# Optimization experiments

Measured on AMD Instinct MI355X. Metric: run time of the kernel, lower is better.

Reference implementation:

```python
import jax, jax.numpy as jnp
import numpy as np

NA, NW = 131072, 131072
N = NA + NW
E = 1048576
R = 4
DIN = 64
H = 128
L = 2
EPS = 1e-5


def setup_inputs() -> dict:
    key = jax.random.key(0)
    ks = jax.random.split(key, 20)
    s_in = 1.0 / np.sqrt(DIN)
    s_h = 1.0 / np.sqrt(H)
    return {
        "x_assignments": jax.random.normal(ks[0], (NA, DIN), jnp.float32),
        "x_workers": jax.random.normal(ks[1], (NW, DIN), jnp.float32),
        "edge_index": jax.random.randint(ks[2], (2, E), 0, N),
        "edge_type": jax.random.randint(ks[3], (E,), 0, R),
        "W_in_a": jax.random.normal(ks[4], (DIN, H), jnp.float32) * s_in,
        "b_in_a": jnp.zeros((H,), jnp.float32),
        "W_in_w": jax.random.normal(ks[5], (DIN, H), jnp.float32) * s_in,
        "b_in_w": jnp.zeros((H,), jnp.float32),
        "W_rel": jax.random.normal(ks[6], (L, R, H, H), jnp.float32) * s_h,
        "W_root": jax.random.normal(ks[7], (L, H, H), jnp.float32) * s_h,
        "b_conv": jnp.zeros((L, H), jnp.float32),
        "ln_g": jnp.ones((L, H), jnp.float32),
        "ln_b": jnp.zeros((L, H), jnp.float32),
        "W_out": jax.random.normal(ks[8], (H, 1), jnp.float32) * s_h,
        "b_out": jnp.zeros((1,), jnp.float32),
        "base": jnp.zeros((), jnp.float32),
    }


def _layernorm(x, g, b):
    mu = jnp.mean(x, axis=-1, keepdims=True)
    var = jnp.var(x, axis=-1, keepdims=True)
    return (x - mu) * jax.lax.rsqrt(var + EPS) * g + b


def reference(x_assignments, x_workers, edge_index, edge_type,
              W_in_a, b_in_a, W_in_w, b_in_w,
              W_rel, W_root, b_conv, ln_g, ln_b,
              W_out, b_out, base):
    # type-specific input projection + relu, then flatten node space
    ha = jax.nn.relu(x_assignments @ W_in_a + b_in_a)
    hw = jax.nn.relu(x_workers @ W_in_w + b_in_w)
    h = jnp.concatenate([ha, hw], axis=0)  # [N, H]
    src, dst = edge_index[0], edge_index[1]
    for l in range(L):
        hs = h[src]  # [E, H] gathered source features
        out = h @ W_root[l] + b_conv[l]  # root transform + bias
        for r in range(R):
            m = (edge_type == r).astype(h.dtype)  # [E]
            agg = jax.ops.segment_sum(hs * m[:, None], dst, num_segments=N)
            cnt = jax.ops.segment_sum(m, dst, num_segments=N)
            mean = agg / jnp.maximum(cnt, 1.0)[:, None]  # per-relation mean aggr
            out = out + mean @ W_rel[l, r]
        h = jax.nn.relu(_layernorm(out, ln_g[l], ln_b[l]))
        # dropout inactive (eval mode)
    h_t = h[:NA]  # target node type slice (offset 0)
    pred = base + (h_t @ W_out + b_out)[:, 0]
    return pred
```

## Files before the change

### kernel.cpp

```cpp
#include <hip/hip_runtime.h>

#define NA_ 131072
#define NN  262144
#define EE  1048576
#define RR  4
#define EPS_ 1e-5f

typedef unsigned short ushort_t;
typedef unsigned char uchar_t;
typedef unsigned int uint_t;
typedef __attribute__((ext_vector_type(8))) short bf16x8;
typedef __attribute__((ext_vector_type(4))) float f32x4;

__device__ __forceinline__ float bf2f(uint_t u16) {
    return __uint_as_float(u16 << 16);
}
__device__ __forceinline__ uint_t f2bf(float f) {
    uint_t x = __float_as_uint(f);
    return (x + 0x7fffu + ((x >> 16) & 1u)) >> 16;
}

__device__ __forceinline__ void gl2lds16(const void* g, void* l) {
    __builtin_amdgcn_global_load_lds(
        (const __attribute__((address_space(1))) void*)g,
        (__attribute__((address_space(3))) void*)l, 16, 0, 0);
}

__global__ __launch_bounds__(256) void proj_gemm(const float* __restrict__ A,
                                                 const short* __restrict__ Btg,
                                                 const float* __restrict__ bias,
                                                 ushort_t* __restrict__ C) {
    const int K = 64;
    __shared__ short As[128][K + 8];
    __shared__ short Bs[128][K + 8];
    const int tid  = threadIdx.x;
    const int lane = tid & 63;
    const int l15  = lane & 15;
    const int q    = lane >> 4;
    const int wv   = tid >> 6;
    const int wr   = (wv >> 1) * 64;
    const int wc   = (wv & 1) * 64;
    const size_t blockRow = (size_t)blockIdx.x * 128;

    #pragma unroll
    for (int it = 0; it < 4; it++) {
        int sidx = (it * 256 + tid) * 8;
        int row = sidx / K, col = sidx % K;
        const float* Ag = A + (blockRow + row) * K + col;
        float4 v0 = *(const float4*)Ag;
        float4 v1 = *(const float4*)(Ag + 4);
        uint4 u;
        u.x = f2bf(v0.x) | (f2bf(v0.y) << 16);
        u.y = f2bf(v0.z) | (f2bf(v0.w) << 16);
        u.z = f2bf(v1.x) | (f2bf(v1.y) << 16);
        u.w = f2bf(v1.z) | (f2bf(v1.w) << 16);
        *(uint4*)&As[row][col] = u;
        *(uint4*)&Bs[row][col] = *(const uint4*)(Btg + (size_t)row * K + col);
    }
    __syncthreads();

    f32x4 acc[4][4];
    #pragma unroll
    for (int i = 0; i < 4; i++)
        #pragma unroll
        for (int j = 0; j < 4; j++) {
            acc[i][j][0] = 0.f; acc[i][j][1] = 0.f;
            acc[i][j][2] = 0.f; acc[i][j][3] = 0.f;
        }

    #pragma unroll
    for (int kk = 0; kk < 2; kk++) {
        bf16x8 af[4], bfr[4];
        #pragma unroll
        for (int i = 0; i < 4; i++)
            af[i] = *(const bf16x8*)&As[wr + i * 16 + l15][kk * 32 + q * 8];
        #pragma unroll
        for (int j = 0; j < 4; j++)
            bfr[j] = *(const bf16x8*)&Bs[wc + j * 16 + l15][kk * 32 + q * 8];
        #pragma unroll
        for (int i = 0; i < 4; i++)
            #pragma unroll
            for (int j = 0; j < 4; j++)
                acc[i][j] = __builtin_amdgcn_mfma_f32_16x16x32_bf16(
                    af[i], bfr[j], acc[i][j], 0, 0, 0);
    }

    #pragma unroll
    for (int j = 0; j < 4; j++) {
        int gcol = wc + j * 16 + l15;
        float bv = bias[gcol];
        #pragma unroll
        for (int i = 0; i < 4; i++) {
            size_t rbase = blockRow + wr + i * 16 + q * 4;
            #pragma unroll
            for (int r = 0; r < 4; r++) {
                float v = fmaxf(acc[i][j][r] + bv, 0.f);
                C[(rbase + r) * 128 + gcol] = (ushort_t)f2bf(v);
            }
        }
    }
}

__global__ void prep_weights(const float* __restrict__ Wia,
                             const float* __restrict__ Wiw,
                             const float* __restrict__ Wroot,
                             const float* __restrict__ Wrel,
                             short* __restrict__ wt) {
    int e = blockIdx.x * 256 + threadIdx.x;
    if (e < 8192) {
        int k = e >> 7, n = e & 127;
        wt[n * 64 + k] = (short)f2bf(Wia[e]);
    } else if (e < 16384) {
        int t = e - 8192;
        int k = t >> 7, n = t & 127;
        wt[8192 + n * 64 + k] = (short)f2bf(Wiw[t]);
    } else {
        int t = e - 16384;
        int l = t / 81920;
        int d = t % 81920;
        int kc = d / 16384;
        int rem2 = d % 16384;
        int n = rem2 >> 7;
        int kkk = rem2 & 127;
        float val = (kc < 4)
            ? Wrel[(((size_t)l * 4 + kc) * 128 + kkk) * 128 + n]
            : Wroot[((size_t)l * 128 + kkk) * 128 + n];
        wt[16384 + (size_t)l * 81920 + kc * 16384 + n * 128 + kkk] =
            (short)f2bf(val);
    }
}

__global__ void count_edges(const int* __restrict__ dstv,
                            const int* __restrict__ et,
                            uint_t* __restrict__ cntp,
                            uchar_t* __restrict__ rank) {
    int base = blockIdx.x * 1024 + threadIdx.x;
    int e0 = base, e1 = base + 256, e2 = base + 512, e3 = base + 768;
    int r0 = et[e0], r1 = et[e1], r2 = et[e2], r3 = et[e3];
    int d0 = dstv[e0], d1 = dstv[e1], d2 = dstv[e2], d3 = dstv[e3];
    uint_t o0 = atomicAdd(&cntp[(size_t)d0 * 16], 1u << (8 * r0));
    uint_t o1 = atomicAdd(&cntp[(size_t)d1 * 16], 1u << (8 * r1));
    uint_t o2 = atomicAdd(&cntp[(size_t)d2 * 16], 1u << (8 * r2));
    uint_t o3 = atomicAdd(&cntp[(size_t)d3 * 16], 1u << (8 * r3));
    rank[e0] = (uchar_t)((o0 >> (8 * r0)) & 0xffu);
    rank[e1] = (uchar_t)((o1 >> (8 * r1)) & 0xffu);
    rank[e2] = (uchar_t)((o2 >> (8 * r2)) & 0xffu);
    rank[e3] = (uchar_t)((o3 >> (8 * r3)) & 0xffu);
}

__global__ void inv_deg(const uint_t* __restrict__ cntp,
                        float* __restrict__ inv,
                        int* __restrict__ deg,
                        uint_t* __restrict__ prefd) {
    int i = blockIdx.x * 256 + threadIdx.x;
    if (i < NN) {
        uint_t c = cntp[(size_t)i * 16];
        int c0 = c & 255, c1 = (c >> 8) & 255, c2 = (c >> 16) & 255, c3 = c >> 24;
        float4 w;
        w.x = 1.0f / (float)(c0 > 1 ? c0 : 1);
        w.y = 1.0f / (float)(c1 > 1 ? c1 : 1);
        w.z = 1.0f / (float)(c2 > 1 ? c2 : 1);
        w.w = 1.0f / (float)(c3 > 1 ? c3 : 1);
        ((float4*)inv)[i] = w;
        deg[i] = c0 + c1 + c2 + c3;
        prefd[i] = ((uint_t)c0 << 8) | ((uint_t)(c0 + c1) << 16)
                 | ((uint_t)(c0 + c1 + c2) << 24);
    }
}

__global__ void scan1(const int* __restrict__ deg, int* __restrict__ offs,
                      int* __restrict__ bsum) {
    __shared__ int lds[256];
    int tid = threadIdx.x;
    int i = blockIdx.x * 256 + tid;
    int v = deg[i];
    int incl = v;
    lds[tid] = incl;
    __syncthreads();
    for (int off = 1; off < 256; off <<= 1) {
        int t = (tid >= off) ? lds[tid - off] : 0;
        __syncthreads();
        incl += t;
        lds[tid] = incl;
        __syncthreads();
    }
    offs[i] = incl - v;
    if (tid == 255) bsum[blockIdx.x] = incl;
}

__global__ void scan_bsum(int* __restrict__ bsum) {
    __shared__ int lds[256];
    int tid = threadIdx.x;
    int t0 = bsum[tid * 4 + 0], t1 = bsum[tid * 4 + 1];
    int t2 = bsum[tid * 4 + 2], t3 = bsum[tid * 4 + 3];
    int s = t0 + t1 + t2 + t3;
    int incl = s;
    lds[tid] = incl;
    __syncthreads();
    for (int off = 1; off < 256; off <<= 1) {
        int t = (tid >= off) ? lds[tid - off] : 0;
        __syncthreads();
        incl += t;
        lds[tid] = incl;
        __syncthreads();
    }
    int e = incl - s;
    bsum[tid * 4 + 0] = e;
    bsum[tid * 4 + 1] = e + t0;
    bsum[tid * 4 + 2] = e + t0 + t1;
    bsum[tid * 4 + 3] = e + t0 + t1 + t2;
}

__global__ void scan_add(int* __restrict__ offs, const int* __restrict__ bsum) {
    int i = blockIdx.x * 256 + threadIdx.x;
    offs[i] = offs[i] + bsum[blockIdx.x];
    if (i == 0) offs[NN] = EE;
}

__global__ void place_edges(const int* __restrict__ srcv,
                            const int* __restrict__ dstv,
                            const int* __restrict__ et,
                            const uchar_t* __restrict__ rank,
                            const int* __restrict__ offs,
                            const uint_t* __restrict__ prefd,
                            uint_t* __restrict__ pk) {
    int base = blockIdx.x * 1024 + threadIdx.x;
    #pragma unroll
    for (int t = 0; t < 4; t++) {
        int e = base + t * 256;
        int d = dstv[e], r = et[e];
        int pos = offs[d] + (int)((prefd[d] >> (8 * r)) & 255u) + (int)rank[e];
        pk[pos] = (uint_t)srcv[e] | ((uint_t)r << 18);
    }
}

__global__ __launch_bounds__(256) void agg_means(const uint_t* __restrict__ pk,
                                                 const int* __restrict__ offs,
                                                 const ushort_t* __restrict__ hold,
                                                 const float* __restrict__ inv,
                                                 ushort_t* __restrict__ M,
                                                 int lo, int rowsCap) {
    const int wv  = __builtin_amdgcn_readfirstlane(threadIdx.x >> 6);
    const int idx = blockIdx.x * 4 + wv;
    const int d   = lo + idx;
    const int lane = threadIdx.x & 63;
    const int beg = offs[d];
    const int end = offs[d + 1];
    const float4 w4 = ((const float4*)inv)[d];

    float a0x = 0.f, a0y = 0.f, a1x = 0.f, a1y = 0.f;
    float a2x = 0.f, a2y = 0.f, a3x = 0.f, a3y = 0.f;

    const uint_t* hold32 = (const uint_t*)hold;

    auto accs = [&](uint_t p, uint_t v, bool valid) {
        float x = bf2f(v & 0xffffu), y = bf2f(v >> 16);
        uint_t r = p >> 18;
        float m0 = (valid && r == 0u) ? 1.f : 0.f;
        float m1 = (valid && r == 1u) ? 1.f : 0.f;
        float m2 = (valid && r == 2u) ? 1.f : 0.f;
        float m3 = (valid && r == 3u) ? 1.f : 0.f;
        a0x += m0 * x;  a0y += m0 * y;
        a1x += m1 * x;  a1y += m1 * y;
        a2x += m2 * x;  a2y += m2 * y;
        a3x += m3 * x;  a3y += m3 * y;
    };

    for (int e = beg; e < end; e += 8) {
        const int last = end - 1;
        int a1i = (e + 1 < end) ? e + 1 : last;
        int a2i = (e + 2 < end) ? e + 2 : last;
        int a3i = (e + 3 < end) ? e + 3 : last;
        uint_t p0 = pk[e];
        uint_t p1 = pk[a1i];
        uint_t p2 = pk[a2i];
        uint_t p3 = pk[a3i];
        uint_t v0 = hold32[(size_t)(p0 & 0x3FFFFu) * 64 + lane];
        uint_t v1 = hold32[(size_t)(p1 & 0x3FFFFu) * 64 + lane];
        uint_t v2 = hold32[(size_t)(p2 & 0x3FFFFu) * 64 + lane];
        uint_t v3 = hold32[(size_t)(p3 & 0x3FFFFu) * 64 + lane];

        const bool hB = (e + 4 < end);
        if (hB) {
            int b1i = (e + 5 < end) ? e + 5 : last;
            int b2i = (e + 6 < end) ? e + 6 : last;
            int b3i = (e + 7 < end) ? e + 7 : last;
            uint_t q0 = pk[e + 4];
            uint_t q1 = pk[b1i];
            uint_t q2 = pk[b2i];
            uint_t q3 = pk[b3i];
            uint_t u0 = hold32[(size_t)(q0 & 0x3FFFFu) * 64 + lane];
            uint_t u1 = hold32[(size_t)(q1 & 0x3FFFFu) * 64 + lane];
            uint_t u2 = hold32[(size_t)(q2 & 0x3FFFFu) * 64 + lane];
            uint_t u3 = hold32[(size_t)(q3 & 0x3FFFFu) * 64 + lane];
            accs(p0, v0, true);
            accs(p1, v1, true);
            accs(p2, v2, true);
            accs(p3, v3, true);
            accs(q0, u0, true);
            accs(q1, u1, e + 5 < end);
            accs(q2, u2, e + 6 < end);
            accs(q3, u3, e + 7 < end);
        } else {
            accs(p0, v0, true);
            accs(p1, v1, e + 1 < end);
            accs(p2, v2, e + 2 < end);
            accs(p3, v3, e + 3 < end);
        }
    }

    uint_t* P = (uint_t*)M;
    size_t planeU = (size_t)rowsCap * 64;
    size_t rowU = (size_t)idx * 64 + lane;
    P[rowU]              = f2bf(a0x * w4.x) | (f2bf(a0y * w4.x) << 16);
    P[planeU + rowU]     = f2bf(a1x * w4.y) | (f2bf(a1y * w4.y) << 16);
    P[2 * planeU + rowU] = f2bf(a2x * w4.z) | (f2bf(a2y * w4.z) << 16);
    P[3 * planeU + rowU] = f2bf(a3x * w4.w) | (f2bf(a3y * w4.w) << 16);
}

template<bool HEAD>
__global__ __launch_bounds__(256) void layer_gemm_ln(
    const ushort_t* __restrict__ Mg,
    const ushort_t* __restrict__ hold,
    const short* __restrict__ Btg,
    const float* __restrict__ bconv,
    const float* __restrict__ lng,
    const float* __restrict__ lnb,
    ushort_t* __restrict__ hnew,
    const float* __restrict__ Wout,
    const float* __restrict__ bout,
    const float* __restrict__ basep,
    float* __restrict__ pred,
    int lo, int rowsCap) {
    __shared__ short As[64 * 128];
    __shared__ short Bs[128 * 128];
    __shared__ float lds_s[64][2], lds_q[64][2], lds_h[64][2];

    const int tid  = threadIdx.x;
    const int lane = tid & 63;
    const int l15  = lane & 15;
    const int q    = lane >> 4;
    const int wv   = tid >> 6;
    const int wr   = (wv >> 1) * 32;
    const int wc   = (wv & 1) * 64;
    const int blockRowL = blockIdx.x * 64;
    const size_t planeS = (size_t)rowsCap * 128;

    f32x4 acc[2][4];
    #pragma unroll
    for (int i = 0; i < 2; i++)
        #pragma unroll
        for (int j = 0; j < 4; j++) {
            acc[i][j][0] = 0.f; acc[i][j][1] = 0.f;
            acc[i][j][2] = 0.f; acc[i][j][3] = 0.f;
        }

    const int rloc = lane >> 4;
    const int gsw  = (lane & 15) ^ ((wv * 4 + rloc) & 15);
    const int lby  = (rloc << 8) + (gsw << 4);

    for (int kc = 0; kc < 5; kc++) {
        const char* asrc = (kc < 4)
            ? (const char*)(Mg + (size_t)kc * planeS + (size_t)blockRowL * 128)
            : (const char*)(hold + (size_t)(lo + blockRowL) * 128);
        const char* bsrc = (const char*)(Btg + (size_t)kc * 16384);
        __syncthreads();
        #pragma unroll
        for (int it = 0; it < 8; it++) {
            int off = it * 4096 + wv * 1024;
            if (it < 4) gl2lds16(asrc + off + lby, (char*)As + off);
            gl2lds16(bsrc + off + lby, (char*)Bs + off);
        }
        __syncthreads();

        #pragma unroll
        for (int kk = 0; kk < 4; kk++) {
            bf16x8 af[2], bfr[4];
            #pragma unroll
            for (int i = 0; i < 2; i++)
                af[i] = *(const bf16x8*)
                    &As[(wr + i * 16 + l15) * 128 + (((kk * 4 + q) ^ l15) << 3)];
            #pragma unroll
            for (int j = 0; j < 4; j++)
                bfr[j] = *(const bf16x8*)
                    &Bs[(wc + j * 16 + l15) * 128 + (((kk * 4 + q) ^ l15) << 3)];
            #pragma unroll
            for (int i = 0; i < 2; i++)
                #pragma unroll
                for (int j = 0; j < 4; j++)
                    acc[i][j] = __builtin_amdgcn_mfma_f32_16x16x32_bf16(
                        af[i], bfr[j], acc[i][j], 0, 0, 0);
        }
    }

    float bj[4], gj[4], bbj[4], wj[4];
    #pragma unroll
    for (int j = 0; j < 4; j++) {
        int col = wc + j * 16 + l15;
        bj[j]  = bconv[col];
        gj[j]  = lng[col];
        bbj[j] = lnb[col];
        if (HEAD) wj[j] = Wout[col];
    }
    #pragma unroll
    for (int i = 0; i < 2; i++)
        #pragma unroll
        for (int j = 0; j < 4; j++)
            #pragma unroll
            for (int r = 0; r < 4; r++) acc[i][j][r] += bj[j];

    float ps[2][4], pq[2][4];
    #pragma unroll
    for (int i = 0; i < 2; i++)
        #pragma unroll
        for (int r = 0; r < 4; r++) {
            float s = 0.f, qq = 0.f;
            #pragma unroll
            for (int j = 0; j < 4; j++) {
                float v = acc[i][j][r];
                s += v;
                qq += v * v;
            }
            ps[i][r] = s;
            pq[i][r] = qq;
        }
    #pragma unroll
    for (int m = 1; m <= 8; m <<= 1)
        #pragma unroll
        for (int i = 0; i < 2; i++)
            #pragma unroll
            for (int r = 0; r < 4; r++) {
                ps[i][r] += __shfl_xor(ps[i][r], m);
                pq[i][r] += __shfl_xor(pq[i][r], m);
            }

    if (l15 == 0) {
        #pragma unroll
        for (int i = 0; i < 2; i++)
            #pragma unroll
            for (int r = 0; r < 4; r++) {
                int row = wr + i * 16 + q * 4 + r;
                lds_s[row][wv & 1] = ps[i][r];
                lds_q[row][wv & 1] = pq[i][r];
            }
    }
    __syncthreads();

    float hs[2][4];
    #pragma unroll
    for (int i = 0; i < 2; i++)
        #pragma unroll
        for (int r = 0; r < 4; r++) {
            int row = wr + i * 16 + q * 4 + r;
            float sum = lds_s[row][0] + lds_s[row][1];
            float sq  = lds_q[row][0] + lds_q[row][1];
            float mu  = sum * (1.0f / 128.0f);
            float var = sq * (1.0f / 128.0f) - mu * mu;
            float rs  = rsqrtf(var + EPS_);
            size_t gr = (size_t)(lo + blockRowL + row) * 128;
            float hd = 0.f;
            #pragma unroll
            for (int j = 0; j < 4; j++) {
                float v = (acc[i][j][r] - mu) * rs * gj[j] + bbj[j];
                v = fmaxf(v, 0.f);
                if (HEAD) hd += v * wj[j];
                else hnew[gr + wc + j * 16 + l15] = (ushort_t)f2bf(v);
            }
            if (HEAD) hs[i][r] = hd;
        }

    if (HEAD) {
        #pragma unroll
        for (int m = 1; m <= 8; m <<= 1)
            #pragma unroll
            for (int i = 0; i < 2; i++)
                #pragma unroll
                for (int r = 0; r < 4; r++)
                    hs[i][r] += __shfl_xor(hs[i][r], m);
        if (l15 == 0) {
            #pragma unroll
            for (int i = 0; i < 2; i++)
                #pragma unroll
                for (int r = 0; r < 4; r++) {
                    int row = wr + i * 16 + q * 4 + r;
                    lds_h[row][wv & 1] = hs[i][r];
                }
        }
        __syncthreads();
        if (tid < 64)
            pred[lo + blockRowL + tid] =
                lds_h[tid][0] + lds_h[tid][1] + bout[0] + basep[0];
    }
}

extern "C" void kernel_launch(void* const* d_in, const int* in_sizes, int n_in,
                              void* d_out, int out_size, void* d_ws, size_t ws_size,
                              hipStream_t stream) {
    const float* x_a    = (const float*)d_in[0];
    const float* x_w    = (const float*)d_in[1];
    const int*   eidx   = (const int*)d_in[2];
    const int*   etype  = (const int*)d_in[3];
    const float* W_in_a = (const float*)d_in[4];
    const float* b_in_a = (const float*)d_in[5];
    const float* W_in_w = (const float*)d_in[6];
    const float* b_in_w = (const float*)d_in[7];
    const float* W_rel  = (const float*)d_in[8];
    const float* W_root = (const float*)d_in[9];
    const float* b_conv = (const float*)d_in[10];
    const float* ln_g   = (const float*)d_in[11];
    const float* ln_b   = (const float*)d_in[12];
    const float* W_out  = (const float*)d_in[13];
    const float* b_out  = (const float*)d_in[14];
    const float* base   = (const float*)d_in[15];

    const int* src  = eidx;
    const int* dstv = eidx + EE;

    char* p = (char*)d_ws;
    auto alloc = [&](size_t bytes) {
        char* q = p;
        p += (bytes + 255) & ~(size_t)255;
        return q;
    };
    ushort_t* hB   = (ushort_t*)alloc((size_t)NN * 128 * 2);
    float*    inv  = (float*)alloc((size_t)RR * NN * 4);
    uint_t*   pk   = (uint_t*)alloc((size_t)EE * 4);
    int*      offs = (int*)alloc((size_t)(NN + 1) * 4);
    short*    wbuf = (short*)alloc((size_t)180224 * 2);
    char*     hA_region = p;
    ushort_t* hA   = (ushort_t*)alloc((size_t)NN * 128 * 2);
    char*     scratch = p;
    uint_t*   cntp  = (uint_t*)alloc((size_t)NN * 64);
    uchar_t*  rank  = (uchar_t*)alloc((size_t)EE);
    int*      deg   = (int*)alloc((size_t)NN * 4);
    uint_t*   prefd = (uint_t*)alloc((size_t)NN * 4);
    int*      bsum  = (int*)alloc((size_t)1024 * 4);

    size_t rem0 = (ws_size > (size_t)(scratch - (char*)d_ws))
                      ? (ws_size - (size_t)(scratch - (char*)d_ws)) : 0;
    int cap0 = (int)(rem0 / 1024);
    if (cap0 > NN) cap0 = NN;
    cap0 &= ~127;
    if (cap0 == 0) cap0 = 128;
    size_t rem1 = (ws_size > (size_t)(hA_region - (char*)d_ws))
                      ? (ws_size - (size_t)(hA_region - (char*)d_ws)) : 0;
    int cap1 = (int)(rem1 / 1024);
    if (cap1 > NA_) cap1 = NA_;
    cap1 &= ~127;
    if (cap1 == 0) cap1 = 128;

    short* wt_ina = wbuf;
    short* wt_inw = wbuf + 8192;
    auto wt_layer = [&](int l) { return wbuf + 16384 + (size_t)l * 81920; };

    hipMemsetAsync(cntp, 0, (size_t)NN * 64, stream);
    count_edges<<<EE / 1024, 256, 0, stream>>>(dstv, etype, cntp, rank);
    inv_deg<<<NN / 256, 256, 0, stream>>>(cntp, inv, deg, prefd);
    scan1<<<NN / 256, 256, 0, stream>>>(deg, offs, bsum);
    scan_bsum<<<1, 256, 0, stream>>>(bsum);
    scan_add<<<NN / 256, 256, 0, stream>>>(offs, bsum);
    place_edges<<<EE / 1024, 256, 0, stream>>>(src, dstv, etype, rank, offs,
                                               prefd, pk);

    prep_weights<<<704, 256, 0, stream>>>(W_in_a, W_in_w, W_root, W_rel, wbuf);

    proj_gemm<<<NA_ / 128, 256, 0, stream>>>(x_a, wt_ina, b_in_a, hA);
    proj_gemm<<<NA_ / 128, 256, 0, stream>>>(x_w, wt_inw, b_in_w,
                                             hA + (size_t)NA_ * 128);

    ushort_t* hc = hA;
    ushort_t* hn = hB;
    for (int l = 0; l < 2; l++) {
        int Nout = (l == 0) ? NN : NA_;
        ushort_t* M = (l == 0) ? (ushort_t*)scratch : (ushort_t*)hA_region;
        int cap = (l == 0) ? cap0 : cap1;
        int nch = (Nout + cap - 1) / cap;
        int chunk = ((Nout / nch) + 127) & ~127;
        if (chunk > cap) chunk = cap;
        for (int lo = 0; lo < Nout; lo += chunk) {
            int cr = (Nout - lo < chunk) ? (Nout - lo) : chunk;
            agg_means<<<cr / 4, 256, 0, stream>>>(pk, offs, hc, inv, M, lo,
                                                  cap);
            if (l == 0)
                layer_gemm_ln<false><<<cr / 64, 256, 0, stream>>>(
                    M, hc, wt_layer(l), b_conv + l * 128, ln_g + l * 128,
                    ln_b + l * 128, hn, nullptr, nullptr, nullptr, nullptr,
                    lo, cap);
            else
                layer_gemm_ln<true><<<cr / 64, 256, 0, stream>>>(
                    M, hc, wt_layer(l), b_conv + l * 128, ln_g + l * 128,
                    ln_b + l * 128, nullptr, W_out, b_out, base,
                    (float*)d_out, lo, cap);
        }
        ushort_t* t = hc; hc = hn; hn = t;
    }
}
```

Measured before the change: 504.5 us.

## Fuse CSR build and weight prep into one cooperative kernel; merge projection GEMMs

Replaces the memset, count, inverse-degree, three-stage scan, edge placement and weight-prep launches with a single cooperative kernel that separates the phases with grid-wide syncs. The two input-projection GEMMs become one launch that picks its operands by block index. The goal is to cut the launch overhead and inter-kernel gaps of many small kernels. The cost is grid.sync barriers, and the design depends on all 1024 blocks being co-resident for the cooperative launch.

```diff
diff --git a/kernel.cpp b/kernel.cpp
--- a/kernel.cpp
+++ b/kernel.cpp
@@ -1,4 +1,7 @@
 #include <hip/hip_runtime.h>
+#include <hip/hip_cooperative_groups.h>
+
+namespace cg = cooperative_groups;
 
 #define NA_ 131072
 #define NN  262144
@@ -26,13 +29,23 @@
         (__attribute__((address_space(3))) void*)l, 16, 0, 0);
 }
 
-__global__ __launch_bounds__(256) void proj_gemm(const float* __restrict__ A,
-                                                 const short* __restrict__ Btg,
-                                                 const float* __restrict__ bias,
-                                                 ushort_t* __restrict__ C) {
+__global__ __launch_bounds__(256) void proj_gemm2(const float* __restrict__ Aa,
+                                                  const float* __restrict__ Aw,
+                                                  const short* __restrict__ Bta,
+                                                  const short* __restrict__ Btw,
+                                                  const float* __restrict__ ba,
+                                                  const float* __restrict__ bw,
+                                                  ushort_t* __restrict__ C) {
     const int K = 64;
     __shared__ short As[128][K + 8];
     __shared__ short Bs[128][K + 8];
+    const bool second = blockIdx.x >= (NA_ / 128);
+    const float* A      = second ? Aw : Aa;
+    const short* Btg    = second ? Btw : Bta;
+    const float* bias   = second ? bw : ba;
+    ushort_t* Cb        = C + (second ? (size_t)NA_ * 128 : 0);
+    const int bidx      = second ? blockIdx.x - NA_ / 128 : blockIdx.x;
+
     const int tid  = threadIdx.x;
     const int lane = tid & 63;
     const int l15  = lane & 15;
@@ -40,7 +53,7 @@
     const int wv   = tid >> 6;
     const int wr   = (wv >> 1) * 64;
     const int wc   = (wv & 1) * 64;
-    const size_t blockRow = (size_t)blockIdx.x * 128;
+    const size_t blockRow = (size_t)bidx * 128;
 
     #pragma unroll
     for (int it = 0; it < 4; it++) {
@@ -95,142 +108,137 @@
             #pragma unroll
             for (int r = 0; r < 4; r++) {
                 float v = fmaxf(acc[i][j][r] + bv, 0.f);
-                C[(rbase + r) * 128 + gcol] = (ushort_t)f2bf(v);
+                Cb[(rbase + r) * 128 + gcol] = (ushort_t)f2bf(v);
             }
         }
     }
 }
 
-__global__ void prep_weights(const float* __restrict__ Wia,
-                             const float* __restrict__ Wiw,
-                             const float* __restrict__ Wroot,
-                             const float* __restrict__ Wrel,
-                             short* __restrict__ wt) {
-    int e = blockIdx.x * 256 + threadIdx.x;
-    if (e < 8192) {
-        int k = e >> 7, n = e & 127;
-        wt[n * 64 + k] = (short)f2bf(Wia[e]);
-    } else if (e < 16384) {
-        int t = e - 8192;
-        int k = t >> 7, n = t & 127;
-        wt[8192 + n * 64 + k] = (short)f2bf(Wiw[t]);
-    } else {
-        int t = e - 16384;
-        int l = t / 81920;
-        int d = t % 81920;
-        int kc = d / 16384;
-        int rem2 = d % 16384;
-        int n = rem2 >> 7;
-        int kkk = rem2 & 127;
-        float val = (kc < 4)
-            ? Wrel[(((size_t)l * 4 + kc) * 128 + kkk) * 128 + n]
-            : Wroot[((size_t)l * 128 + kkk) * 128 + n];
-        wt[16384 + (size_t)l * 81920 + kc * 16384 + n * 128 + kkk] =
-            (short)f2bf(val);
-    }
-}
-
-__global__ void count_edges(const int* __restrict__ dstv,
-                            const int* __restrict__ et,
-                            uint_t* __restrict__ cntp,
-                            uchar_t* __restrict__ rank) {
-    int base = blockIdx.x * 1024 + threadIdx.x;
-    int e0 = base, e1 = base + 256, e2 = base + 512, e3 = base + 768;
-    int r0 = et[e0], r1 = et[e1], r2 = et[e2], r3 = et[e3];
-    int d0 = dstv[e0], d1 = dstv[e1], d2 = dstv[e2], d3 = dstv[e3];
-    uint_t o0 = atomicAdd(&cntp[(size_t)d0 * 16], 1u << (8 * r0));
-    uint_t o1 = atomicAdd(&cntp[(size_t)d1 * 16], 1u << (8 * r1));
-    uint_t o2 = atomicAdd(&cntp[(size_t)d2 * 16], 1u << (8 * r2));
-    uint_t o3 = atomicAdd(&cntp[(size_t)d3 * 16], 1u << (8 * r3));
-    rank[e0] = (uchar_t)((o0 >> (8 * r0)) & 0xffu);
-    rank[e1] = (uchar_t)((o1 >> (8 * r1)) & 0xffu);
-    rank[e2] = (uchar_t)((o2 >> (8 * r2)) & 0xffu);
-    rank[e3] = (uchar_t)((o3 >> (8 * r3)) & 0xffu);
-}
-
-__global__ void inv_deg(const uint_t* __restrict__ cntp,
-                        float* __restrict__ inv,
-                        int* __restrict__ deg,
-                        uint_t* __restrict__ prefd) {
-    int i = blockIdx.x * 256 + threadIdx.x;
-    if (i < NN) {
-        uint_t c = cntp[(size_t)i * 16];
+__global__ __launch_bounds__(256) void csr_build(
+    const int* __restrict__ dstv, const int* __restrict__ et,
+    const int* __restrict__ srcv,
+    const float* __restrict__ Wia, const float* __restrict__ Wiw,
+    const float* __restrict__ Wroot, const float* __restrict__ Wrel,
+    uint_t* __restrict__ cntp, uchar_t* __restrict__ rank,
+    float* __restrict__ inv, uint_t* __restrict__ prefd,
+    int* __restrict__ offs, int* __restrict__ bsum,
+    uint_t* __restrict__ pk, short* __restrict__ wt) {
+    cg::grid_group grid = cg::this_grid();
+    __shared__ int lds[256];
+    const int tid = threadIdx.x;
+    const int bid = blockIdx.x;
+    const int gt  = bid * 256 + tid;
+
+    cntp[(size_t)gt * 16] = 0u;
+    {
+        int e = gt;
+        if (e < 8192) {
+            int k = e >> 7, n = e & 127;
+            wt[n * 64 + k] = (short)f2bf(Wia[e]);
+        } else if (e < 16384) {
+            int t = e - 8192;
+            int k = t >> 7, n = t & 127;
+            wt[8192 + n * 64 + k] = (short)f2bf(Wiw[t]);
+        } else if (e < 180224) {
+            int t = e - 16384;
+            int l = t / 81920;
+            int d = t % 81920;
+            int kc = d / 16384;
+            int rem2 = d % 16384;
+            int n = rem2 >> 7;
+            int kkk = rem2 & 127;
+            float val = (kc < 4)
+                ? Wrel[(((size_t)l * 4 + kc) * 128 + kkk) * 128 + n]
+                : Wroot[((size_t)l * 128 + kkk) * 128 + n];
+            wt[16384 + (size_t)l * 81920 + kc * 16384 + n * 128 + kkk] =
+                (short)f2bf(val);
+        }
+    }
+    grid.sync();
+
+    {
+        int base = bid * 1024 + tid;
+        int e0 = base, e1 = base + 256, e2 = base + 512, e3 = base + 768;
+        int r0 = et[e0], r1 = et[e1], r2 = et[e2], r3 = et[e3];
+        int d0 = dstv[e0], d1 = dstv[e1], d2 = dstv[e2], d3 = dstv[e3];
+        uint_t o0 = atomicAdd(&cntp[(size_t)d0 * 16], 1u << (8 * r0));
+        uint_t o1 = atomicAdd(&cntp[(size_t)d1 * 16], 1u << (8 * r1));
+        uint_t o2 = atomicAdd(&cntp[(size_t)d2 * 16], 1u << (8 * r2));
+        uint_t o3 = atomicAdd(&cntp[(size_t)d3 * 16], 1u << (8 * r3));
+        rank[e0] = (uchar_t)((o0 >> (8 * r0)) & 0xffu);
+        rank[e1] = (uchar_t)((o1 >> (8 * r1)) & 0xffu);
+        rank[e2] = (uchar_t)((o2 >> (8 * r2)) & 0xffu);
+        rank[e3] = (uchar_t)((o3 >> (8 * r3)) & 0xffu);
+    }
+    grid.sync();
+
+    int mydeg;
+    {
+        uint_t c = cntp[(size_t)gt * 16];
         int c0 = c & 255, c1 = (c >> 8) & 255, c2 = (c >> 16) & 255, c3 = c >> 24;
         float4 w;
         w.x = 1.0f / (float)(c0 > 1 ? c0 : 1);
         w.y = 1.0f / (float)(c1 > 1 ? c1 : 1);
         w.z = 1.0f / (float)(c2 > 1 ? c2 : 1);
         w.w = 1.0f / (float)(c3 > 1 ? c3 : 1);
-        ((float4*)inv)[i] = w;
-        deg[i] = c0 + c1 + c2 + c3;
-        prefd[i] = ((uint_t)c0 << 8) | ((uint_t)(c0 + c1) << 16)
-                 | ((uint_t)(c0 + c1 + c2) << 24);
-    }
-}
-
-__global__ void scan1(const int* __restrict__ deg, int* __restrict__ offs,
-                      int* __restrict__ bsum) {
-    __shared__ int lds[256];
-    int tid = threadIdx.x;
-    int i = blockIdx.x * 256 + tid;
-    int v = deg[i];
-    int incl = v;
-    lds[tid] = incl;
-    __syncthreads();
-    for (int off = 1; off < 256; off <<= 1) {
-        int t = (tid >= off) ? lds[tid - off] : 0;
-        __syncthreads();
-        incl += t;
+        ((float4*)inv)[gt] = w;
+        mydeg = c0 + c1 + c2 + c3;
+        prefd[gt] = ((uint_t)c0 << 8) | ((uint_t)(c0 + c1) << 16)
+                  | ((uint_t)(c0 + c1 + c2) << 24);
+    }
+
+    {
+        int incl = mydeg;
         lds[tid] = incl;
         __syncthreads();
-    }
-    offs[i] = incl - v;
-    if (tid == 255) bsum[blockIdx.x] = incl;
-}
-
-__global__ void scan_bsum(int* __restrict__ bsum) {
-    __shared__ int lds[256];
-    int tid = threadIdx.x;
-    int t0 = bsum[tid * 4 + 0], t1 = bsum[tid * 4 + 1];
-    int t2 = bsum[tid * 4 + 2], t3 = bsum[tid * 4 + 3];
-    int s = t0 + t1 + t2 + t3;
-    int incl = s;
-    lds[tid] = incl;
-    __syncthreads();
-    for (int off = 1; off < 256; off <<= 1) {
-        int t = (tid >= off) ? lds[tid - off] : 0;
-        __syncthreads();
-        incl += t;
+        for (int off = 1; off < 256; off <<= 1) {
+            int t = (tid >= off) ? lds[tid - off] : 0;
+            __syncthreads();
+            incl += t;
+            lds[tid] = incl;
+            __syncthreads();
+        }
+        offs[gt] = incl - mydeg;
+        if (tid == 255) bsum[bid] = incl;
+    }
+    grid.sync();
+
+    if (bid == 0) {
+        int t0 = bsum[tid * 4 + 0], t1 = bsum[tid * 4 + 1];
+        int t2 = bsum[tid * 4 + 2], t3 = bsum[tid * 4 + 3];
+        int s = t0 + t1 + t2 + t3;
+        int incl = s;
         lds[tid] = incl;
         __syncthreads();
-    }
-    int e = incl - s;
-    bsum[tid * 4 + 0] = e;
-    bsum[tid * 4 + 1] = e + t0;
-    bsum[tid * 4 + 2] = e + t0 + t1;
-    bsum[tid * 4 + 3] = e + t0 + t1 + t2;
-}
-
-__global__ void scan_add(int* __restrict__ offs, const int* __restrict__ bsum) {
-    int i = blockIdx.x * 256 + threadIdx.x;
-    offs[i] = offs[i] + bsum[blockIdx.x];
-    if (i == 0) offs[NN] = EE;
-}
-
-__global__ void place_edges(const int* __restrict__ srcv,
-                            const int* __restrict__ dstv,
-                            const int* __restrict__ et,
-                            const uchar_t* __restrict__ rank,
-                            const int* __restrict__ offs,
-                            const uint_t* __restrict__ prefd,
-                            uint_t* __restrict__ pk) {
-    int base = blockIdx.x * 1024 + threadIdx.x;
-    #pragma unroll
-    for (int t = 0; t < 4; t++) {
-        int e = base + t * 256;
-        int d = dstv[e], r = et[e];
-        int pos = offs[d] + (int)((prefd[d] >> (8 * r)) & 255u) + (int)rank[e];
-        pk[pos] = (uint_t)srcv[e] | ((uint_t)r << 18);
+        for (int off = 1; off < 256; off <<= 1) {
+            int t = (tid >= off) ? lds[tid - off] : 0;
+            __syncthreads();
+            incl += t;
+            lds[tid] = incl;
+            __syncthreads();
+        }
+        int e = incl - s;
+        bsum[tid * 4 + 0] = e;
+        bsum[tid * 4 + 1] = e + t0;
+        bsum[tid * 4 + 2] = e + t0 + t1;
+        bsum[tid * 4 + 3] = e + t0 + t1 + t2;
+    }
+    grid.sync();
+
+    offs[gt] = offs[gt] + bsum[bid];
+    if (gt == 0) offs[NN] = EE;
+    grid.sync();
+
+    {
+        int base = bid * 1024 + tid;
+        #pragma unroll
+        for (int t = 0; t < 4; t++) {
+            int e = base + t * 256;
+            int d = dstv[e], r = et[e];
+            int pos = offs[d] + (int)((prefd[d] >> (8 * r)) & 255u)
+                    + (int)rank[e];
+            pk[pos] = (uint_t)srcv[e] | ((uint_t)r << 18);
+        }
     }
 }
 
@@ -532,7 +540,6 @@
     char*     scratch = p;
     uint_t*   cntp  = (uint_t*)alloc((size_t)NN * 64);
     uchar_t*  rank  = (uchar_t*)alloc((size_t)EE);
-    int*      deg   = (int*)alloc((size_t)NN * 4);
     uint_t*   prefd = (uint_t*)alloc((size_t)NN * 4);
     int*      bsum  = (int*)alloc((size_t)1024 * 4);
 
@@ -553,20 +560,19 @@
     short* wt_inw = wbuf + 8192;
     auto wt_layer = [&](int l) { return wbuf + 16384 + (size_t)l * 81920; };
 
-    hipMemsetAsync(cntp, 0, (size_t)NN * 64, stream);
-    count_edges<<<EE / 1024, 256, 0, stream>>>(dstv, etype, cntp, rank);
-    inv_deg<<<NN / 256, 256, 0, stream>>>(cntp, inv, deg, prefd);
-    scan1<<<NN / 256, 256, 0, stream>>>(deg, offs, bsum);
-    scan_bsum<<<1, 256, 0, stream>>>(bsum);
-    scan_add<<<NN / 256, 256, 0, stream>>>(offs, bsum);
-    place_edges<<<EE / 1024, 256, 0, stream>>>(src, dstv, etype, rank, offs,
-                                               prefd, pk);
-
-    prep_weights<<<704, 256, 0, stream>>>(W_in_a, W_in_w, W_root, W_rel, wbuf);
-
-    proj_gemm<<<NA_ / 128, 256, 0, stream>>>(x_a, wt_ina, b_in_a, hA);
-    proj_gemm<<<NA_ / 128, 256, 0, stream>>>(x_w, wt_inw, b_in_w,
-                                             hA + (size_t)NA_ * 128);
+    {
+        void* cargs[] = {
+            (void*)&dstv, (void*)&etype, (void*)&src,
+            (void*)&W_in_a, (void*)&W_in_w, (void*)&W_root, (void*)&W_rel,
+            (void*)&cntp, (void*)&rank, (void*)&inv, (void*)&prefd,
+            (void*)&offs, (void*)&bsum, (void*)&pk, (void*)&wbuf
+        };
+        hipLaunchCooperativeKernel((const void*)csr_build, dim3(1024),
+                                   dim3(256), cargs, 0, stream);
+    }
+
+    proj_gemm2<<<2 * (NA_ / 128), 256, 0, stream>>>(
+        x_a, x_w, wt_ina, wt_inw, b_in_a, b_in_w, hA);
 
     ushort_t* hc = hA;
     ushort_t* hn = hB;
```

Result: slower. 1.018 ms (+101.7%).
